# Optimization experiments

Hardware: AMD Instinct MI355X
Metric: run time of the kernel (lower is better)

The kernel has to match this reference:

```python
import jax, jax.numpy as jnp
import numpy as np
from jax import lax

THRE = 0.01
K_SIZE = 5
C_SIGMA = 1.0
VOXEL = 0.4          # args['voxel_size'][0] -> discrete_ratio
DOWNSAMPLE = 4       # args['downsample_rate']


def gaussian_kernel(k=K_SIZE, sigma=C_SIGMA):
    c = k // 2
    gx, gy = np.mgrid[-c:k - c, -c:k - c]
    g = 1.0 / (2.0 * np.pi * sigma) * np.exp(-(gx ** 2 + gy ** 2) / (2.0 * sigma ** 2))
    return jnp.asarray(g, dtype=jnp.float32)


def affine_grid(theta, H, W):
    # theta: [N,2,3]; matches F.affine_grid(align_corners=False)
    dt = theta.dtype
    xs = (jnp.arange(W, dtype=dt) + 0.5) * (2.0 / W) - 1.0
    ys = (jnp.arange(H, dtype=dt) + 0.5) * (2.0 / H) - 1.0
    xg, yg = jnp.meshgrid(xs, ys)                      # [H,W]
    base = jnp.stack([xg, yg, jnp.ones_like(xg)], -1)  # [H,W,3]
    return jnp.einsum('hwk,nck->nhwc', base, theta)    # [N,H,W,2] (x_s, y_s)


def grid_sample_bilinear(src, grid):
    # src [N,C,H,W], grid [N,H,W,2] in [-1,1]; bilinear, zeros padding, align_corners=False
    N, C, H, W = src.shape
    x = ((grid[..., 0] + 1.0) * W - 1.0) * 0.5
    y = ((grid[..., 1] + 1.0) * H - 1.0) * 0.5
    x0f = jnp.floor(x)
    y0f = jnp.floor(y)
    wx1 = x - x0f
    wy1 = y - y0f

    def sample_one(src_n, x0f_n, y0f_n, wx1_n, wy1_n):
        x0 = x0f_n.astype(jnp.int32)
        y0 = y0f_n.astype(jnp.int32)

        def gather(ix, iy):
            valid = ((ix >= 0) & (ix < W) & (iy >= 0) & (iy < H)).astype(src.dtype)
            ixc = jnp.clip(ix, 0, W - 1)
            iyc = jnp.clip(iy, 0, H - 1)
            return src_n[:, iyc, ixc] * valid[None]    # [C,H,W]

        g00 = gather(x0, y0)
        g01 = gather(x0 + 1, y0)
        g10 = gather(x0, y0 + 1)
        g11 = gather(x0 + 1, y0 + 1)
        wx0 = 1.0 - wx1_n
        wy0 = 1.0 - wy1_n
        return (g00 * (wx0 * wy0)[None] + g01 * (wx1_n * wy0)[None]
                + g10 * (wx0 * wy1_n)[None] + g11 * (wx1_n * wy1_n)[None])

    return jax.vmap(sample_one)(src, x0f, y0f, wx1, wy1)


def atten_fuse(feat):
    # feat: [N,C,H,W]; per-pixel scaled-dot-product attention over agents, keep ego row.
    N, C, H, W = feat.shape
    seq = feat.reshape(N, C, H * W).transpose(2, 0, 1)          # [HW, N, C]
    q0 = seq[:, 0, :]                                           # ego query [HW, C]
    score = jnp.einsum('pc,pnc->pn', q0, seq) / np.sqrt(C)      # row 0 of NxN scores
    attn = jax.nn.softmax(score, axis=-1)
    ctx = jnp.einsum('pn,pnc->pc', attn, seq)                   # [HW, C]
    return ctx.T.reshape(C, H, W)


def _forward(x, psm_single, pairwise_t_matrix):
    B, L = pairwise_t_matrix.shape[:2]
    _, C, H, W = x.shape
    A = psm_single.shape[1]

    # ---- normalize 4x4 transforms to 2x3 affine matrices (as in Where2comm.forward)
    t = pairwise_t_matrix[..., :2, :][..., jnp.array([0, 1, 3])]   # [B,L,L,2,3]
    t = t.at[..., 0, 1].multiply(H / W)
    t = t.at[..., 1, 0].multiply(W / H)
    t = t.at[..., 0, 2].set(t[..., 0, 2] / (DOWNSAMPLE * VOXEL * W) * 2.0)
    t = t.at[..., 1, 2].set(t[..., 1, 2] / (DOWNSAMPLE * VOXEL * H) * 2.0)

    # ---- Communication: confidence -> gaussian smooth -> threshold mask
    conf = jnp.max(jax.nn.sigmoid(psm_single), axis=1, keepdims=True)  # [B*L,1,H,W]
    gk = gaussian_kernel()
    pad = (K_SIZE - 1) // 2
    smoothed = lax.conv_general_dilated(
        conf, gk[None, None], (1, 1), [(pad, pad), (pad, pad)],
        dimension_numbers=('NCHW', 'OIHW', 'NCHW'))
    mask = (smoothed > THRE).astype(x.dtype)                            # [B*L,1,H,W]
    mask = mask.reshape(B, L, 1, H, W)
    mask = mask.at[:, ::2].set(1.0)                                     # nodiag trick per batch
    rate = jnp.mean(jnp.sum(mask[:, 0], axis=(1, 2, 3)) / (H * W))

    # ---- mask features, warp every agent into ego frame, attention-fuse
    xm = x.reshape(B, L, C, H, W) * mask[:, :, :, :, :]                 # broadcast over C

    def fuse_scene(feat_b, t_b):
        # feat_b: [L,C,H,W]; t_b: [L,L,2,3]; ego row of transforms warps all agents to ego
        grid = affine_grid(t_b[0], H, W)                                # [L,H,W,2]
        neighbor = grid_sample_bilinear(feat_b, grid)                   # [L,C,H,W]
        return atten_fuse(neighbor)                                     # [C,H,W]

    x_fuse = jax.vmap(fuse_scene)(xm, t)                                # [B,C,H,W]
    return x_fuse, rate


def setup_inputs() -> dict:
    key = jax.random.key(0)
    B, L, C, A, H, W = 2, 5, 256, 2, 100, 252
    k1, k2, k3 = jax.random.split(key, 3)
    x = jax.random.normal(k1, (B * L, C, H, W), jnp.float32)
    psm_single = jax.random.normal(k2, (B * L, A, H, W), jnp.float32)
    # near-identity 4x4 pose transforms with small random translations (meters)
    t = jnp.tile(jnp.eye(4, dtype=jnp.float32), (B, L, L, 1, 1))
    trans = jax.random.uniform(k3, (B, L, L, 2), jnp.float32, -10.0, 10.0)
    t = t.at[..., 0, 3].set(trans[..., 0])
    t = t.at[..., 1, 3].set(trans[..., 1])
    idx = jnp.arange(L)
    t = t.at[:, idx, idx].set(jnp.eye(4, dtype=jnp.float32))  # self-transform = identity
    record_len = jnp.full((B,), L, dtype=jnp.int32)
    return {"x": x, "psm_single": psm_single, "pairwise_t_matrix": t, "record_len": record_len}


def reference(x, psm_single, pairwise_t_matrix, record_len):
    x_fuse, rate = _forward(x, psm_single, pairwise_t_matrix)
    return x_fuse
```

## Files before the change

### kernel.cpp

```cpp
#include <hip/hip_runtime.h>
#include <math.h>

#define BB 2
#define LL 5
#define CC 256
#define HH 100
#define WW 252
#define HW (HH*WW)
#define CHW (CC*HW)
#define THRE_F 0.01f

typedef float v2f __attribute__((ext_vector_type(2)));
typedef float v4f __attribute__((ext_vector_type(4)));

__device__ __forceinline__ v2f ld2v(const float* p) {
    v2f v; __builtin_memcpy(&v, p, 8); return v;
}
__device__ __forceinline__ v4f ld4v(const float* p) {
    v4f v; __builtin_memcpy(&v, p, 16); return v;
}
__device__ __forceinline__ void st2v(float* p, v2f v) {
    __builtin_memcpy(p, &v, 8);
}
__device__ __forceinline__ float dot8(const float* c, v4f A, v4f B) {
    return c[0]*A.x + c[1]*A.y + c[2]*A.z + c[3]*A.w
         + c[4]*B.x + c[5]*B.y + c[6]*B.z + c[7]*B.w;
}

__device__ const float GW[5][5] = {
    {0.002915024f, 0.013064233f, 0.021539279f, 0.013064233f, 0.002915024f},
    {0.013064233f, 0.058549832f, 0.096532353f, 0.058549832f, 0.013064233f},
    {0.021539279f, 0.096532353f, 0.159154943f, 0.096532353f, 0.021539279f},
    {0.013064233f, 0.058549832f, 0.096532353f, 0.058549832f, 0.013064233f},
    {0.002915024f, 0.013064233f, 0.021539279f, 0.013064233f, 0.002915024f},
};

__global__ void mask_kernel(const float* __restrict__ psm, float* __restrict__ mask)
{
    int idx = blockIdx.x * blockDim.x + threadIdx.x;
    if (idx >= 4 * HW) return;
    int m = idx / HW;
    int p = idx - m * HW;
    int h = p / WW;
    int w = p - h * WW;
    int n = (m >> 1) * LL + ((m & 1) * 2 + 1);
    const float* base0 = psm + (size_t)n * 2 * HW;
    const float* base1 = base0 + HW;

    float acc = 0.0f;
#pragma unroll
    for (int i = 0; i < 5; ++i) {
        int yy = h + i - 2;
        if (yy < 0 || yy >= HH) continue;
#pragma unroll
        for (int j = 0; j < 5; ++j) {
            int xx = w + j - 2;
            if (xx < 0 || xx >= WW) continue;
            float v = fmaxf(base0[yy * WW + xx], base1[yy * WW + xx]);
            acc += GW[i][j] / (1.0f + __expf(-v));
        }
    }
    mask[idx] = (acc > THRE_F) ? 1.0f : 0.0f;
}

struct XF { float t00, t01, t02, t10, t11, t12; };

__device__ __forceinline__ XF load_xf(const float* __restrict__ pt, int b, int l) {
    const float* M = pt + (size_t)(b * LL * LL + l) * 16;
    XF X;
    X.t00 = M[0];
    X.t01 = M[1] * (100.0f / 252.0f);
    X.t02 = M[3] / 403.2f * 2.0f;
    X.t10 = M[4] * (252.0f / 100.0f);
    X.t11 = M[5];
    X.t12 = M[7] / 160.0f * 2.0f;
    return X;
}
__device__ __forceinline__ bool is_trans(const XF& X) {
    return X.t00 == 1.0f && X.t01 == 0.0f && X.t10 == 0.0f && X.t11 == 1.0f;
}

__device__ __forceinline__ void setup_trans(
    int l, int b, int h, int px0, float act, const XF& X,
    const float* __restrict__ maskw, int cstart,
    float cf[16], int o2[2])
{
    float tx = X.t02 * (WW * 0.5f);
    float ty = X.t12 * (HH * 0.5f);
    int ix = (int)floorf(tx);
    int iy = (int)floorf(ty);
    float wx1 = tx - (float)ix, wx0 = 1.0f - wx1;
    float wy1 = ty - (float)iy, wy0 = 1.0f - wy1;
    int y0 = h + iy, y1 = y0 + 1;
    int cy0 = min(max(y0, 0), HH - 1), cy1 = min(max(y1, 0), HH - 1);
    float vy0 = (y0 >= 0 && y0 < HH) ? 1.0f : 0.0f;
    float vy1 = (y1 >= 0 && y1 < HH) ? 1.0f : 0.0f;

    int craw = px0 + ix;
    int col = craw & ~1;
    col = min(max(col, 0), WW - 4);
    int d = craw - col;

    const float* mb = nullptr;
    if (l & 1) mb = maskw + (size_t)(b * 2 + (l >> 1)) * HW;

#pragma unroll
    for (int k = 0; k < 16; ++k) cf[k] = 0.0f;
#pragma unroll
    for (int px = 0; px < 2; ++px) {
#pragma unroll
        for (int r = 0; r < 2; ++r) {
#pragma unroll
            for (int t = 0; t < 2; ++t) {
                int xt = craw + px + t;
                float vx  = (xt >= 0 && xt < WW) ? 1.0f : 0.0f;
                float wcol = t ? wx1 : wx0;
                float wrow = r ? wy1 : wy0;
                float vyw  = r ? vy1 : vy0;
                float m = 1.0f;
                if (mb) {
                    int cx = min(max(xt, 0), WW - 1);
                    int cy = r ? cy1 : cy0;
                    m = mb[cy * WW + cx];
                }
                float wgt = wcol * wrow * vyw * vx * m * act;
                int e = d + px + t;
#pragma unroll
                for (int k = 0; k < 4; ++k)
                    if (e == k) cf[px * 8 + r * 4 + k] += wgt;
            }
        }
    }
    int nbase = (b * LL + l) * CHW + cstart * HW;
    o2[0] = nbase + cy0 * WW + col;
    o2[1] = nbase + cy1 * WW + col;
}

__device__ __forceinline__ void setup_gen(
    int l, int b, int h, int px0, float act, const XF& X,
    const float* __restrict__ maskw, int cstart,
    float gc[8], int o4[4])
{
    const float* mb = nullptr;
    if (l & 1) mb = maskw + (size_t)(b * 2 + (l >> 1)) * HW;
    float ysn = (h + 0.5f) * (2.0f / HH) - 1.0f;
    int nbase = (b * LL + l) * CHW + cstart * HW;

#pragma unroll
    for (int px = 0; px < 2; ++px) {
        float xsn = (px0 + px + 0.5f) * (2.0f / WW) - 1.0f;
        float gx = X.t00 * xsn + X.t01 * ysn + X.t02;
        float gy = X.t10 * xsn + X.t11 * ysn + X.t12;
        float fx = ((gx + 1.0f) * WW - 1.0f) * 0.5f;
        float fy = ((gy + 1.0f) * HH - 1.0f) * 0.5f;
        float fx0 = floorf(fx), fy0 = floorf(fy);
        float wx1 = fx - fx0, wy1 = fy - fy0;
        float wx0 = 1.0f - wx1, wy0 = 1.0f - wy1;
        int x0 = (int)fx0, y0 = (int)fy0;
        int x1 = x0 + 1, y1 = y0 + 1;
        int cx0 = min(max(x0, 0), WW - 1), cx1 = min(max(x1, 0), WW - 1);
        int cy0 = min(max(y0, 0), HH - 1), cy1 = min(max(y1, 0), HH - 1);
        float vx0 = (x0 >= 0 && x0 < WW) ? 1.0f : 0.0f;
        float vx1 = (x1 >= 0 && x1 < WW) ? 1.0f : 0.0f;
        float vy0 = (y0 >= 0 && y0 < HH) ? 1.0f : 0.0f;
        float vy1 = (y1 >= 0 && y1 < HH) ? 1.0f : 0.0f;
        float m00 = 1, m01 = 1, m10 = 1, m11 = 1;
        if (mb) {
            m00 = mb[cy0 * WW + cx0]; m01 = mb[cy0 * WW + cx1];
            m10 = mb[cy1 * WW + cx0]; m11 = mb[cy1 * WW + cx1];
        }
        float w00 = wx0 * wy0 * vx0 * vy0 * m00 * act;
        float w01 = wx1 * wy0 * vx1 * vy0 * m01 * act;
        float w10 = wx0 * wy1 * vx0 * vy1 * m10 * act;
        float w11 = wx1 * wy1 * vx1 * vy1 * m11 * act;
        int bx = min(max(x0, 0), WW - 2);
        int dd = x0 - bx;
        gc[px * 4 + 0] = (dd == 0 ? w00 : 0.f) + (dd == -1 ? w01 : 0.f);
        gc[px * 4 + 1] = (dd == 0 ? w01 : 0.f) + (dd ==  1 ? w00 : 0.f);
        gc[px * 4 + 2] = (dd == 0 ? w10 : 0.f) + (dd == -1 ? w11 : 0.f);
        gc[px * 4 + 3] = (dd == 0 ? w11 : 0.f) + (dd ==  1 ? w10 : 0.f);
        o4[px * 2 + 0] = nbase + cy0 * WW + bx;
        o4[px * 2 + 1] = nbase + cy1 * WW + bx;
    }
}

__global__ __launch_bounds__(256) void score_kernel(
    const float* __restrict__ x, const float* __restrict__ pt,
    const float* __restrict__ maskw, float* __restrict__ scoresP)
{
    int blk = blockIdx.x;
    int cc = blk & 1;
    int wt = (blk >> 1) & 1;
    int t  = blk >> 2;
    int h  = t % HH;
    int b  = t / HH;

    int tid = threadIdx.x;
    int lane = tid & 63;
    int cg   = tid >> 6;
    int px0  = wt * 128 + 2 * lane;
    float act = (px0 < WW) ? 1.0f : 0.0f;
    v2f act2 = {act, act};
    int cstart = cc * 128 + cg * 32;

    XF X[LL];
#pragma unroll
    for (int l = 0; l < LL; ++l) X[l] = load_xf(pt, b, l);
    bool ident0 = is_trans(X[0]) && X[0].t02 == 0.0f && X[0].t12 == 0.0f;
    bool ftrans = ident0 && is_trans(X[1]) && is_trans(X[2])
                         && is_trans(X[3]) && is_trans(X[4]);

    v2f s[LL];
#pragma unroll
    for (int l = 0; l < LL; ++l) s[l] = (v2f){0.f, 0.f};

    if (ftrans) {
        int f0off = b * LL * CHW + cstart * HW + h * WW + min(px0, WW - 2);
        float cf[4][16];
        int o[8];
#pragma unroll
        for (int l = 1; l < LL; ++l)
            setup_trans(l, b, h, px0, act, X[l], maskw, cstart, cf[l - 1], &o[(l - 1) * 2]);

        for (int ci = 0; ci < 32; ++ci) {
            v2f f0 = ld2v(x + f0off) * act2;  f0off += HW;
            s[0] += f0 * f0;
#pragma unroll
            for (int l = 1; l < LL; ++l) {
                v4f F0 = ld4v(x + o[(l - 1) * 2 + 0]);
                v4f F1 = ld4v(x + o[(l - 1) * 2 + 1]);
                o[(l - 1) * 2 + 0] += HW;
                o[(l - 1) * 2 + 1] += HW;
                v2f fl;
                fl.x = dot8(&cf[l - 1][0], F0, F1);
                fl.y = dot8(&cf[l - 1][8], F0, F1);
                s[l] += f0 * fl;
            }
        }
    } else {
        float gc[LL][8];
        int go[LL][4];
#pragma unroll
        for (int l = 0; l < LL; ++l)
            setup_gen(l, b, h, px0, act, X[l], maskw, cstart, gc[l], go[l]);

        for (int ci = 0; ci < 32; ++ci) {
            v2f fv[LL];
#pragma unroll
            for (int l = 0; l < LL; ++l) {
                v2f R00 = ld2v(x + go[l][0]);
                v2f R01 = ld2v(x + go[l][1]);
                v2f R10 = ld2v(x + go[l][2]);
                v2f R11 = ld2v(x + go[l][3]);
#pragma unroll
                for (int k = 0; k < 4; ++k) go[l][k] += HW;
                fv[l].x = gc[l][0]*R00.x + gc[l][1]*R00.y + gc[l][2]*R01.x + gc[l][3]*R01.y;
                fv[l].y = gc[l][4]*R10.x + gc[l][5]*R10.y + gc[l][6]*R11.x + gc[l][7]*R11.y;
            }
#pragma unroll
            for (int l = 0; l < LL; ++l) s[l] += fv[0] * fv[l];
        }
    }

    __shared__ v2f sred[4][LL][64];
#pragma unroll
    for (int l = 0; l < LL; ++l) sred[cg][l][lane] = s[l];
    __syncthreads();

    if (tid < 64 && px0 < WW) {
        int p = h * WW + px0;
#pragma unroll
        for (int l = 0; l < LL; ++l) {
            v2f v = (sred[0][l][lane] + sred[1][l][lane]
                   + sred[2][l][lane] + sred[3][l][lane]) * 0.0625f;
            st2v(&scoresP[((cc * BB + b) * LL + l) * HW + p], v);
        }
    }
}

__global__ __launch_bounds__(256) void out_kernel(
    const float* __restrict__ x, const float* __restrict__ pt,
    const float* __restrict__ maskw, const float* __restrict__ scoresP,
    float* __restrict__ out)
{
    int blk = blockIdx.x;
    int cc = blk & 1;
    int wt = (blk >> 1) & 1;
    int t  = blk >> 2;
    int h  = t % HH;
    int b  = t / HH;

    int tid = threadIdx.x;
    int lane = tid & 63;
    int cg   = tid >> 6;
    int px0  = wt * 128 + 2 * lane;
    float act = (px0 < WW) ? 1.0f : 0.0f;
    v2f act2 = {act, act};
    int cstart = cc * 128 + cg * 32;

    v2f a[LL];
    {
        int p = min(h * WW + px0, HW - 2);
        v2f mx = {-1e30f, -1e30f};
#pragma unroll
        for (int l = 0; l < LL; ++l) {
            v2f sc = ld2v(scoresP + (b * LL + l) * HW + p)
                   + ld2v(scoresP + ((BB + b) * LL + l) * HW + p);
            a[l] = sc;
            mx.x = fmaxf(mx.x, sc.x);
            mx.y = fmaxf(mx.y, sc.y);
        }
        v2f denom = {0.f, 0.f};
#pragma unroll
        for (int l = 0; l < LL; ++l) {
            a[l].x = __expf(a[l].x - mx.x);
            a[l].y = __expf(a[l].y - mx.y);
            denom += a[l];
        }
        v2f inv = {1.0f / denom.x, 1.0f / denom.y};
#pragma unroll
        for (int l = 0; l < LL; ++l) a[l] *= inv;
    }

    XF X[LL];
#pragma unroll
    for (int l = 0; l < LL; ++l) X[l] = load_xf(pt, b, l);
    bool ident0 = is_trans(X[0]) && X[0].t02 == 0.0f && X[0].t12 == 0.0f;
    bool ftrans = ident0 && is_trans(X[1]) && is_trans(X[2])
                         && is_trans(X[3]) && is_trans(X[4]);

    int obase = b * CHW + cstart * HW + h * WW + px0;
    bool doStore = (px0 < WW);

    if (ftrans) {
        int f0off = b * LL * CHW + cstart * HW + h * WW + min(px0, WW - 2);
        float cf[4][16];
        int o[8];
#pragma unroll
        for (int l = 1; l < LL; ++l) {
            setup_trans(l, b, h, px0, act, X[l], maskw, cstart, cf[l - 1], &o[(l - 1) * 2]);
#pragma unroll
            for (int k = 0; k < 8; ++k) {
                cf[l - 1][k]     *= a[l].x;
                cf[l - 1][k + 8] *= a[l].y;
            }
        }
        v2f af0 = a[0] * act2;

        for (int ci = 0; ci < 32; ++ci) {
            v2f f0 = ld2v(x + f0off);  f0off += HW;
            v2f ctx = af0 * f0;
#pragma unroll
            for (int l = 1; l < LL; ++l) {
                v4f F0 = ld4v(x + o[(l - 1) * 2 + 0]);
                v4f F1 = ld4v(x + o[(l - 1) * 2 + 1]);
                o[(l - 1) * 2 + 0] += HW;
                o[(l - 1) * 2 + 1] += HW;
                ctx.x += dot8(&cf[l - 1][0], F0, F1);
                ctx.y += dot8(&cf[l - 1][8], F0, F1);
            }
            if (doStore) st2v(&out[obase], ctx);
            obase += HW;
        }
    } else {
        float gc[LL][8];
        int go[LL][4];
#pragma unroll
        for (int l = 0; l < LL; ++l) {
            setup_gen(l, b, h, px0, act, X[l], maskw, cstart, gc[l], go[l]);
#pragma unroll
            for (int k = 0; k < 4; ++k) {
                gc[l][k]     *= a[l].x;
                gc[l][k + 4] *= a[l].y;
            }
        }
        for (int ci = 0; ci < 32; ++ci) {
            v2f ctx = {0.f, 0.f};
#pragma unroll
            for (int l = 0; l < LL; ++l) {
                v2f R00 = ld2v(x + go[l][0]);
                v2f R01 = ld2v(x + go[l][1]);
                v2f R10 = ld2v(x + go[l][2]);
                v2f R11 = ld2v(x + go[l][3]);
#pragma unroll
                for (int k = 0; k < 4; ++k) go[l][k] += HW;
                ctx.x += gc[l][0]*R00.x + gc[l][1]*R00.y + gc[l][2]*R01.x + gc[l][3]*R01.y;
                ctx.y += gc[l][4]*R10.x + gc[l][5]*R10.y + gc[l][6]*R11.x + gc[l][7]*R11.y;
            }
            if (doStore) st2v(&out[obase], ctx);
            obase += HW;
        }
    }
}

extern "C" void kernel_launch(void* const* d_in, const int* in_sizes, int n_in,
                              void* d_out, int out_size, void* d_ws, size_t ws_size,
                              hipStream_t stream)
{
    const float* x   = (const float*)d_in[0];
    const float* psm = (const float*)d_in[1];
    const float* pt  = (const float*)d_in[2];
    float* out = (float*)d_out;

    float* maskw  = (float*)d_ws;
    float* scores = maskw + 4 * HW;

    mask_kernel<<<(4 * HW + 255) / 256, 256, 0, stream>>>(psm, maskw);
    score_kernel<<<BB * HH * 2 * 2, 256, 0, stream>>>(x, pt, maskw, scores);
    out_kernel<<<BB * HH * 2 * 2, 256, 0, stream>>>(x, pt, maskw, scores, out);
}
```

Before: 502.7 us.

## Split channels into four chunks, swizzle blocks across XCDs, add occupancy hint

Measured after the change: 484.1 us. 1.04x faster.

```diff
diff --git a/kernel.cpp b/kernel.cpp
--- a/kernel.cpp
+++ b/kernel.cpp
@@ -10,6 +10,9 @@
 #define CHW (CC*HW)
 #define THRE_F 0.01f
 
+#define NCC 4
+#define CI_PER_CG 16
+
 typedef float v2f __attribute__((ext_vector_type(2)));
 typedef float v4f __attribute__((ext_vector_type(4)));
 
@@ -25,6 +28,11 @@
 __device__ __forceinline__ float dot8(const float* c, v4f A, v4f B) {
     return c[0]*A.x + c[1]*A.y + c[2]*A.z + c[3]*A.w
          + c[4]*B.x + c[5]*B.y + c[6]*B.z + c[7]*B.w;
+}
+
+__device__ __forceinline__ int xcd_swizzle(int blk, int nblk) {
+    int q = nblk >> 3;
+    return (blk & 7) * q + (blk >> 3);
 }
 
 __device__ const float GW[5][5] = {
@@ -184,14 +192,14 @@
     }
 }
 
-__global__ __launch_bounds__(256) void score_kernel(
+__global__ __launch_bounds__(256, 4) void score_kernel(
     const float* __restrict__ x, const float* __restrict__ pt,
     const float* __restrict__ maskw, float* __restrict__ scoresP)
 {
-    int blk = blockIdx.x;
-    int cc = blk & 1;
-    int wt = (blk >> 1) & 1;
-    int t  = blk >> 2;
+    int blk = xcd_swizzle(blockIdx.x, gridDim.x);
+    int cc = blk & (NCC - 1);
+    int wt = (blk >> 2) & 1;
+    int t  = blk >> 3;
     int h  = t % HH;
     int b  = t / HH;
 
@@ -201,7 +209,7 @@
     int px0  = wt * 128 + 2 * lane;
     float act = (px0 < WW) ? 1.0f : 0.0f;
     v2f act2 = {act, act};
-    int cstart = cc * 128 + cg * 32;
+    int cstart = cc * (CC / NCC) + cg * CI_PER_CG;
 
     XF X[LL];
 #pragma unroll
@@ -222,7 +230,7 @@
         for (int l = 1; l < LL; ++l)
             setup_trans(l, b, h, px0, act, X[l], maskw, cstart, cf[l - 1], &o[(l - 1) * 2]);
 
-        for (int ci = 0; ci < 32; ++ci) {
+        for (int ci = 0; ci < CI_PER_CG; ++ci) {
             v2f f0 = ld2v(x + f0off) * act2;  f0off += HW;
             s[0] += f0 * f0;
 #pragma unroll
@@ -244,7 +252,7 @@
         for (int l = 0; l < LL; ++l)
             setup_gen(l, b, h, px0, act, X[l], maskw, cstart, gc[l], go[l]);
 
-        for (int ci = 0; ci < 32; ++ci) {
+        for (int ci = 0; ci < CI_PER_CG; ++ci) {
             v2f fv[LL];
 #pragma unroll
             for (int l = 0; l < LL; ++l) {
@@ -278,15 +286,15 @@
     }
 }
 
-__global__ __launch_bounds__(256) void out_kernel(
+__global__ __launch_bounds__(256, 4) void out_kernel(
     const float* __restrict__ x, const float* __restrict__ pt,
     const float* __restrict__ maskw, const float* __restrict__ scoresP,
     float* __restrict__ out)
 {
-    int blk = blockIdx.x;
-    int cc = blk & 1;
-    int wt = (blk >> 1) & 1;
-    int t  = blk >> 2;
+    int blk = xcd_swizzle(blockIdx.x, gridDim.x);
+    int cc = blk & (NCC - 1);
+    int wt = (blk >> 2) & 1;
+    int t  = blk >> 3;
     int h  = t % HH;
     int b  = t / HH;
 
@@ -296,7 +304,7 @@
     int px0  = wt * 128 + 2 * lane;
     float act = (px0 < WW) ? 1.0f : 0.0f;
     v2f act2 = {act, act};
-    int cstart = cc * 128 + cg * 32;
+    int cstart = cc * (CC / NCC) + cg * CI_PER_CG;
 
     v2f a[LL];
     {
@@ -304,8 +312,10 @@
         v2f mx = {-1e30f, -1e30f};
 #pragma unroll
         for (int l = 0; l < LL; ++l) {
-            v2f sc = ld2v(scoresP + (b * LL + l) * HW + p)
-                   + ld2v(scoresP + ((BB + b) * LL + l) * HW + p);
+            v2f sc = {0.f, 0.f};
+#pragma unroll
+            for (int q = 0; q < NCC; ++q)
+                sc += ld2v(scoresP + ((q * BB + b) * LL + l) * HW + p);
             a[l] = sc;
             mx.x = fmaxf(mx.x, sc.x);
             mx.y = fmaxf(mx.y, sc.y);
@@ -347,7 +357,7 @@
         }
         v2f af0 = a[0] * act2;
 
-        for (int ci = 0; ci < 32; ++ci) {
+        for (int ci = 0; ci < CI_PER_CG; ++ci) {
             v2f f0 = ld2v(x + f0off);  f0off += HW;
             v2f ctx = af0 * f0;
 #pragma unroll
@@ -374,7 +384,7 @@
                 gc[l][k + 4] *= a[l].y;
             }
         }
-        for (int ci = 0; ci < 32; ++ci) {
+        for (int ci = 0; ci < CI_PER_CG; ++ci) {
             v2f ctx = {0.f, 0.f};
 #pragma unroll
             for (int l = 0; l < LL; ++l) {
@@ -406,6 +416,6 @@
     float* scores = maskw + 4 * HW;
 
     mask_kernel<<<(4 * HW + 255) / 256, 256, 0, stream>>>(psm, maskw);
-    score_kernel<<<BB * HH * 2 * 2, 256, 0, stream>>>(x, pt, maskw, scores);
-    out_kernel<<<BB * HH * 2 * 2, 256, 0, stream>>>(x, pt, maskw, scores, out);
-}
+    score_kernel<<<BB * HH * 2 * NCC, 256, 0, stream>>>(x, pt, maskw, scores);
+    out_kernel<<<BB * HH * 2 * NCC, 256, 0, stream>>>(x, pt, maskw, scores, out);
+}
```
